# Kernel tuning notes

Measured on AMD Instinct MI355X. Metric: run time of the kernel, lower is better.

## Reference

```python
import jax, jax.numpy as jnp
import numpy as np

Q_DIM = 1024
KV_DIM = 1024
D_ATTN = 1024
N_HEADS = 16
HDIM = D_ATTN // N_HEADS
LOOKBACK = 3
KW = LOOKBACK + 1
SCALE = HDIM ** -0.5

B, LQ, LKV = 4, 4096, 512


def setup_inputs() -> dict:
    key = jax.random.key(0)
    ks = jax.random.split(key, 6)
    q = jax.random.normal(ks[0], (B, LQ, Q_DIM), dtype=jnp.float32)
    kv_src = jax.random.normal(ks[1], (B, LKV, KV_DIM), dtype=jnp.float32)
    seg_id = jnp.sort(jax.random.randint(ks[2], (B, LQ), 0, LKV), axis=-1)
    # Linear weights (torch convention: y = x @ W.T), no bias
    Wq = jax.random.normal(ks[3], (D_ATTN, Q_DIM), dtype=jnp.float32) * (Q_DIM ** -0.5)
    Wkv = jax.random.normal(ks[4], (2 * D_ATTN, KV_DIM), dtype=jnp.float32) * (KV_DIM ** -0.5)
    Wo = jax.random.normal(ks[5], (Q_DIM, D_ATTN), dtype=jnp.float32) * (D_ATTN ** -0.5)
    return {"q": q, "kv_src": kv_src, "seg_id": seg_id, "Wq": Wq, "Wkv": Wkv, "Wo": Wo}


def _split_heads(x):
    # (B, L, D) -> (B, H, L, Dh)
    b, l, _ = x.shape
    return x.reshape(b, l, N_HEADS, HDIM).transpose(0, 2, 1, 3)


def reference(q, kv_src, seg_id, Wq, Wkv, Wo):
    b, lq, _ = q.shape
    lkv = kv_src.shape[1]

    qh = _split_heads(q @ Wq.T)                      # (B,H,Lq,Dh)
    kv = kv_src @ Wkv.T                              # (B,Lkv,2*D)
    k, v = jnp.split(kv, 2, axis=-1)
    kh = _split_heads(k)                             # (B,H,Lkv,Dh)
    vh = _split_heads(v)

    offsets = jnp.arange(KW)                         # (Kw,)
    gather = seg_id[:, :, None] - offsets            # (B,Lq,Kw)
    neg_mask = gather < 0
    gc = jnp.clip(gather, 0, lkv - 1)                # (B,Lq,Kw)

    b_idx = jnp.arange(b)[:, None, None]
    # advanced indexing: (B,Lq,Kw,H,Dh) -> transpose to (B,H,Lq,Kw,Dh)
    k_sel = kh[b_idx, :, gc].transpose(0, 3, 1, 2, 4)
    v_sel = vh[b_idx, :, gc].transpose(0, 3, 1, 2, 4)

    scores = jnp.einsum('bhqd,bhqkd->bhqk', qh, k_sel) * SCALE
    neg_inf = jnp.finfo(scores.dtype).min
    scores = jnp.where(neg_mask[:, None, :, :], neg_inf, scores)
    probs = jax.nn.softmax(scores, axis=-1)
    out = jnp.einsum('bhqk,bhqkd->bhqd', probs, v_sel)   # (B,H,Lq,Dh)
    out = out.transpose(0, 2, 1, 3).reshape(b, lq, D_ATTN)
    return out @ Wo.T                                # (B,Lq,q_dim)
```

## Files before the change

kernel.cpp:

```cpp
#include <hip/hip_runtime.h>
#include <math.h>

#define NH 16
#define HDIM 64
#define D_ATTN 1024
#define KW 4
#define ATT_SCALE 0.125f
#define LKV_C 512
#define LQ_C 4096
#define B_C 4

typedef _Float16 f16;
typedef _Float16 f16x8 __attribute__((ext_vector_type(8)));
typedef _Float16 f16x4 __attribute__((ext_vector_type(4)));
typedef float f32x4 __attribute__((ext_vector_type(4)));

typedef __attribute__((address_space(3))) unsigned int as3_uint;
typedef __attribute__((address_space(1))) const unsigned int as1_uint;

__device__ __forceinline__ void gld_lds16(const f16* g, f16* l) {
    __builtin_amdgcn_global_load_lds((as1_uint*)g, (as3_uint*)l, 16, 0, 0);
}

#define SEG_Q   4194304
#define SEG_KV  (SEG_Q + 524288)
#define SEG_WQ  (SEG_KV + 262144)
#define SEG_WKV (SEG_WQ + 524288)
#define SEG_END (SEG_WKV + 262144)

__global__ __launch_bounds__(256) void split_all(const float* __restrict__ q,
                                                 const float* __restrict__ kv,
                                                 const float* __restrict__ Wq,
                                                 const float* __restrict__ Wkv,
                                                 const float* __restrict__ Wo,
                                                 f16* __restrict__ q_hi,
                                                 f16* __restrict__ kvs_hi,
                                                 f16* __restrict__ Wq_hi,
                                                 f16* __restrict__ Wkv_hi,
                                                 f16* __restrict__ Wo_hi) {
    const int i = blockIdx.x * 256 + threadIdx.x;
    const float* src; f16* dst; int base;
    if (i < SEG_Q)        { src = q;   dst = q_hi;   base = 0; }
    else if (i < SEG_KV)  { src = kv;  dst = kvs_hi; base = SEG_Q; }
    else if (i < SEG_WQ)  { src = Wq;  dst = Wq_hi;  base = SEG_KV; }
    else if (i < SEG_WKV) { src = Wkv; dst = Wkv_hi; base = SEG_WQ; }
    else                  { src = Wo;  dst = Wo_hi;  base = SEG_WKV; }
    const int j = i - base;
    float4 v = ((const float4*)src)[j];
    ((f16x4*)dst)[j] = (f16x4){(f16)v.x, (f16)v.y, (f16)v.z, (f16)v.w};
}

template <typename OT>
__global__ __launch_bounds__(256) void gemm_f16(const f16* __restrict__ A,
                                                const f16* __restrict__ B,
                                                OT* __restrict__ C,
                                                int M, int N, int K) {
    __shared__ f16 smem[2 * 128 * 32];
    f16* sA = smem;
    f16* sB = smem + 4096;

    const int t = threadIdx.x;
    const int w = t >> 6;
    const int lane = t & 63;
    const int bm = blockIdx.y * 128;
    const int bn = blockIdx.x * 128;
    const int wm = (w & 1) * 64;
    const int wn = (w >> 1) * 64;

    f32x4 acc[4][4] = {};

    const int frow = lane & 15;
    const int fchunk = lane >> 4;

    const int srow = t >> 2;
    const int chunk = (t & 3) ^ ((t >> 3) & 3);
    const size_t aoff0 = (size_t)(bm + srow) * K + chunk * 8;
    const size_t aoff1 = (size_t)(bm + 64 + srow) * K + chunk * 8;
    const size_t boff0 = (size_t)(bn + srow) * K + chunk * 8;
    const size_t boff1 = (size_t)(bn + 64 + srow) * K + chunk * 8;
    const unsigned loff0 = (w * 64) * 8;
    const unsigned loff1 = (256 + w * 64) * 8;

    gld_lds16(A + aoff0, sA + loff0);  gld_lds16(A + aoff1, sA + loff1);
    gld_lds16(B + boff0, sB + loff0);  gld_lds16(B + boff1, sB + loff1);

    for (int k0 = 0; k0 < K; k0 += 32) {
        __syncthreads();

        f16x8 a[4], b[4];
        #pragma unroll
        for (int i = 0; i < 4; ++i) {
            const int r = wm + i * 16 + frow;
            a[i] = *(const f16x8*)(sA + r * 32 + (fchunk ^ ((r >> 1) & 3)) * 8);
        }
        #pragma unroll
        for (int j = 0; j < 4; ++j) {
            const int r = wn + j * 16 + frow;
            b[j] = *(const f16x8*)(sB + r * 32 + (fchunk ^ ((r >> 1) & 3)) * 8);
        }

        __syncthreads();

        if (k0 + 32 < K) {
            const int kn = k0 + 32;
            gld_lds16(A + aoff0 + kn, sA + loff0);  gld_lds16(A + aoff1 + kn, sA + loff1);
            gld_lds16(B + boff0 + kn, sB + loff0);  gld_lds16(B + boff1 + kn, sB + loff1);
        }

        #pragma unroll
        for (int i = 0; i < 4; ++i)
            #pragma unroll
            for (int j = 0; j < 4; ++j)
                acc[i][j] = __builtin_amdgcn_mfma_f32_16x16x32_f16(a[i], b[j], acc[i][j], 0, 0, 0);
    }

    const int rbase = bm + wm + (lane >> 4) * 4;
    const int cbase = bn + wn + (lane & 15);
    #pragma unroll
    for (int i = 0; i < 4; ++i)
        #pragma unroll
        for (int j = 0; j < 4; ++j)
            #pragma unroll
            for (int r = 0; r < 4; ++r)
                C[(size_t)(rbase + i * 16 + r) * N + cbase + j * 16] = (OT)acc[i][j][r];
}

__device__ __forceinline__ void stage64(const f16* __restrict__ g, size_t row0,
                                        int K, int kcol, f16* l) {
    const int t = threadIdx.x;
    #pragma unroll
    for (int i = 0; i < 2; ++i) {
        const int idx = i * 256 + t;
        const int r = idx >> 3;
        const int qg = (idx & 7) ^ (r & 7);
        gld_lds16(g + (row0 + r) * (size_t)K + kcol + qg * 8, l + idx * 8);
    }
}

#define BAR __builtin_amdgcn_s_barrier()
#define VM6 asm volatile("s_waitcnt vmcnt(6)" ::: "memory")
#define VM8 asm volatile("s_waitcnt vmcnt(8)" ::: "memory")
#define VM0 asm volatile("s_waitcnt vmcnt(0)" ::: "memory")

#define RD_A(S, mh)                                                         \
    { _Pragma("unroll") for (int mi = 0; mi < 2; ++mi) {                    \
        const f16* p = (S) + ((mh) * 64 + mi * 32 + arow) * 64;             \
        a[0][mi] = *(const f16x8*)(p + q0);                                 \
        a[1][mi] = *(const f16x8*)(p + q1); } }

#define RD_B(S, nh)                                                         \
    { _Pragma("unroll") for (int ni = 0; ni < 2; ++ni) {                    \
        const f16* p = (S) + (((nh) * 2 + ni) * 32 + brow) * 64;            \
        b[0][(nh) * 2 + ni] = *(const f16x8*)(p + q0);                      \
        b[1][(nh) * 2 + ni] = *(const f16x8*)(p + q1); } }

#define QUAD(mh, nh)                                                        \
    { _Pragma("unroll") for (int mi = 0; mi < 2; ++mi)                      \
      _Pragma("unroll") for (int ni = 0; ni < 2; ++ni) {                    \
          f32x4& c = acc[(mh) * 2 + mi][(nh) * 2 + ni];                     \
          c = __builtin_amdgcn_mfma_f32_16x16x32_f16(a[0][mi], b[0][(nh) * 2 + ni], c, 0, 0, 0); \
          c = __builtin_amdgcn_mfma_f32_16x16x32_f16(a[1][mi], b[1][(nh) * 2 + ni], c, 0, 0, 0); \
      } }

#define QUAD2(mh)                                                           \
    { __builtin_amdgcn_s_setprio(1); QUAD(mh, 0); QUAD(mh, 1);              \
      __builtin_amdgcn_s_setprio(0); }

template <typename OT>
__global__ __launch_bounds__(256, 2) void gemm128(const f16* __restrict__ A,
                                                  const f16* __restrict__ B,
                                                  OT* __restrict__ C,
                                                  int M, int N, int K) {
    __shared__ __align__(16) f16 smem[4 * 8192];
    f16* const sA0 = smem;
    f16* const sA1 = smem + 8192;
    f16* const sB0 = smem + 16384;
    f16* const sB1 = smem + 24576;

    const int t = threadIdx.x;
    const int lane = t & 63;
    const int w = t >> 6;
    const int wr = w >> 1;
    const int wc = w & 1;
    const int frow = lane & 15;
    const int fc = lane >> 4;

    const int nbx = N >> 7;
    const int nwg = gridDim.x;
    const int wg = (blockIdx.x & 7) * (nwg >> 3) + (blockIdx.x >> 3);
    const int bm = (wg / nbx) << 7;
    const int bn = (wg % nbx) << 7;

    const int arow = wr * 16 + frow;
    const int brow = wc * 16 + frow;
    const int q0 = (fc ^ (frow & 7)) * 8;
    const int q1 = ((4 + fc) ^ (frow & 7)) * 8;

    f32x4 acc[4][4] = {};
    f16x8 a[2][2], b[2][4];

    stage64(A, bm,      K, 0,  sA0);
    stage64(A, bm + 64, K, 0,  sA0 + 4096);
    stage64(B, bn,      K, 0,  sB0);
    stage64(B, bn + 64, K, 0,  sB0 + 4096);
    stage64(A, bm,      K, 64, sA1);
    stage64(A, bm + 64, K, 64, sA1 + 4096);
    stage64(B, bn,      K, 64, sB1);
    stage64(B, bn + 64, K, 64, sB1 + 4096);
    VM8;
    BAR;

    const int NT = K >> 7;
    for (int it = 0; it < NT; ++it) {
        const bool lastit = (it == NT - 1);
        const int kc1 = (it * 2 + 1) << 6;
        const int kc2 = (it * 2 + 2) << 6;
        const int kc3 = (it * 2 + 3) << 6;

        RD_A(sA0, 0); RD_B(sB0, 0); RD_B(sB0, 1);
        if (it > 0) stage64(A, bm + 64, K, kc1, sA1 + 4096);
        BAR; QUAD2(0); BAR;

        RD_A(sA0, 1);
        if (!lastit) {
            stage64(A, bm,      K, kc2, sA0);
            stage64(B, bn,      K, kc2, sB0);
            stage64(B, bn + 64, K, kc2, sB0 + 4096);
            VM6;
        } else {
            VM0;
        }
        BAR; QUAD2(1); BAR;

        RD_A(sA1, 0); RD_B(sB1, 0); RD_B(sB1, 1);
        if (!lastit) stage64(A, bm + 64, K, kc2, sA0 + 4096);
        BAR; QUAD2(0); BAR;

        RD_A(sA1, 1);
        if (!lastit) {
            stage64(A, bm,      K, kc3, sA1);
            stage64(B, bn,      K, kc3, sB1);
            stage64(B, bn + 64, K, kc3, sB1 + 4096);
            VM6;
        }
        BAR; QUAD2(1); BAR;
    }

    const size_t rb = (size_t)bm + wr * 16 + ((lane >> 4) << 2);
    const int cb = bn + wc * 16 + (lane & 15);
    #pragma unroll
    for (int m = 0; m < 4; ++m)
        #pragma unroll
        for (int n = 0; n < 4; ++n)
            #pragma unroll
            for (int rr = 0; rr < 4; ++rr)
                C[(rb + (m >> 1) * 64 + (m & 1) * 32 + rr) * N + cb + n * 32] =
                    (OT)acc[m][n][rr];
}

__global__ __launch_bounds__(256) void attn_kernel(const f16* __restrict__ qh,
                                                   const f16* __restrict__ kvp,
                                                   const int* __restrict__ seg_id,
                                                   f16* __restrict__ attn_o) {
    const int hg = threadIdx.x >> 6;
    const int lane = threadIdx.x & 63;
    const int r0 = blockIdx.x << 2;
    const int hh = lane >> 4;
    const int s  = lane & 15;
    const int dbase = (hg * 4 + hh) * HDIM + 4 * s;
    const int b = r0 >> 12;
    const f16* kvb = kvp + (size_t)b * LKV_C * (2 * D_ATTN);

    int seg[4];
    float4 q[4];
    #pragma unroll
    for (int i = 0; i < 4; ++i) {
        seg[i] = seg_id[r0 + i];
        f16x4 qv = *(const f16x4*)(qh + (size_t)(r0 + i) * D_ATTN + dbase);
        q[i] = make_float4((float)qv.x, (float)qv.y, (float)qv.z, (float)qv.w);
    }

    float sc[4][KW];
    #pragma unroll
    for (int i = 0; i < 4; ++i)
        #pragma unroll
        for (int w = 0; w < KW; ++w) {
            const int j = seg[i] - w;
            float p = 0.f;
            if (j >= 0) {
                f16x4 k4 = *(const f16x4*)(kvb + (size_t)j * (2 * D_ATTN) + dbase);
                p = q[i].x * (float)k4.x + q[i].y * (float)k4.y +
                    q[i].z * (float)k4.z + q[i].w * (float)k4.w;
            }
            sc[i][w] = p;
        }
    #pragma unroll
    for (int i = 0; i < 4; ++i)
        #pragma unroll
        for (int w = 0; w < KW; ++w) {
            float p = sc[i][w];
            p += __shfl_xor(p, 1);
            p += __shfl_xor(p, 2);
            p += __shfl_xor(p, 4);
            p += __shfl_xor(p, 8);
            sc[i][w] = (seg[i] - w >= 0) ? p * ATT_SCALE : -1e30f;
        }

    #pragma unroll
    for (int i = 0; i < 4; ++i) {
        const float m = fmaxf(fmaxf(sc[i][0], sc[i][1]), fmaxf(sc[i][2], sc[i][3]));
        float e[KW], sum = 0.f;
        #pragma unroll
        for (int w = 0; w < KW; ++w) {
            e[w] = __expf(sc[i][w] - m);
            sum += e[w];
        }
        const float inv = 1.f / sum;

        float4 o = make_float4(0.f, 0.f, 0.f, 0.f);
        #pragma unroll
        for (int w = 0; w < KW; ++w) {
            const int j = seg[i] - w;
            if (j >= 0) {
                f16x4 v4 = *(const f16x4*)(kvb + (size_t)j * (2 * D_ATTN) + D_ATTN + dbase);
                const float c = e[w] * inv;
                o.x = fmaf(c, (float)v4.x, o.x);
                o.y = fmaf(c, (float)v4.y, o.y);
                o.z = fmaf(c, (float)v4.z, o.z);
                o.w = fmaf(c, (float)v4.w, o.w);
            }
        }
        *(f16x4*)(attn_o + (size_t)(r0 + i) * D_ATTN + dbase) =
            (f16x4){(f16)o.x, (f16)o.y, (f16)o.z, (f16)o.w};
    }
}

extern "C" void kernel_launch(void* const* d_in, const int* in_sizes, int n_in,
                              void* d_out, int out_size, void* d_ws, size_t ws_size,
                              hipStream_t stream) {
    const float* q      = (const float*)d_in[0];
    const float* kv_src = (const float*)d_in[1];
    const int*   seg    = (const int*)  d_in[2];
    const float* Wq     = (const float*)d_in[3];
    const float* Wkv    = (const float*)d_in[4];
    const float* Wo     = (const float*)d_in[5];
    float* out = (float*)d_out;

    const int M  = B_C * LQ_C;
    const int Mk = B_C * LKV_C;

    f16* q_hi   = (f16*)d_ws;
    f16* kvs_hi = q_hi   + (size_t)M * D_ATTN;
    f16* Wq_hi  = kvs_hi + (size_t)Mk * 1024;
    f16* Wkv_hi = Wq_hi  + 1024 * 1024;
    f16* Wo_hi  = Wkv_hi + 2048 * 1024;
    f16* kvp    = Wo_hi  + 1024 * 1024;
    f16* attn_o = q_hi;
    f16* qh16   = (f16*)d_out;

    split_all<<<SEG_END / 256, 256, 0, stream>>>(q, kv_src, Wq, Wkv, Wo,
                                                 q_hi, kvs_hi, Wq_hi, Wkv_hi, Wo_hi);

    gemm_f16<f16><<<dim3(2048 / 128, Mk / 128), 256, 0, stream>>>(kvs_hi, Wkv_hi, kvp, Mk, 2048, 1024);
    gemm128<f16><<<(M / 128) * (1024 / 128), 256, 0, stream>>>(q_hi, Wq_hi, qh16, M, 1024, 1024);
    attn_kernel<<<M / 4, 256, 0, stream>>>(qh16, kvp, seg, attn_o);
    gemm128<float><<<(M / 128) * (1024 / 128), 256, 0, stream>>>(attn_o, Wo_hi, out, M, 1024, 1024);
}
```

Baseline: 266.8 us.

## Fuse local-window attention into the Q-projection GEMM epilogue

The Q-projection GEMM now stages its 128x128 output tile in shared memory. It then runs the 4-key windowed attention (dot products via fdot2, softmax, and the weighted V sum) for its two heads directly in the epilogue, writing the attention output to a separate workspace buffer. This removes the separate attention kernel and the round trip of qh through global memory. In exchange, the GEMM blocks carry a longer, latency-bound epilogue with scattered KV gathers. The old path remains as a fallback when the workspace is too small.

```diff
diff --git a/kernel.cpp b/kernel.cpp
--- a/kernel.cpp
+++ b/kernel.cpp
@@ -13,6 +13,7 @@
 typedef _Float16 f16;
 typedef _Float16 f16x8 __attribute__((ext_vector_type(8)));
 typedef _Float16 f16x4 __attribute__((ext_vector_type(4)));
+typedef _Float16 f16x2 __attribute__((ext_vector_type(2)));
 typedef float f32x4 __attribute__((ext_vector_type(4)));
 
 typedef __attribute__((address_space(3))) unsigned int as3_uint;
@@ -20,6 +21,18 @@
 
 __device__ __forceinline__ void gld_lds16(const f16* g, f16* l) {
     __builtin_amdgcn_global_load_lds((as1_uint*)g, (as3_uint*)l, 16, 0, 0);
+}
+
+__device__ __forceinline__ float dot4_f16(f16x4 a, f16x4 b) {
+#if __has_builtin(__builtin_amdgcn_fdot2)
+    f16x2 alo = {a.x, a.y}, ahi = {a.z, a.w};
+    f16x2 blo = {b.x, b.y}, bhi = {b.z, b.w};
+    float p = __builtin_amdgcn_fdot2(alo, blo, 0.f, false);
+    return __builtin_amdgcn_fdot2(ahi, bhi, p, false);
+#else
+    return (float)a.x * (float)b.x + (float)a.y * (float)b.y +
+           (float)a.z * (float)b.z + (float)a.w * (float)b.w;
+#endif
 }
 
 #define SEG_Q   4194304
@@ -166,11 +179,13 @@
     { __builtin_amdgcn_s_setprio(1); QUAD(mh, 0); QUAD(mh, 1);              \
       __builtin_amdgcn_s_setprio(0); }
 
-template <typename OT>
+template <typename OT, bool FUSE>
 __global__ __launch_bounds__(256, 2) void gemm128(const f16* __restrict__ A,
                                                   const f16* __restrict__ B,
                                                   OT* __restrict__ C,
-                                                  int M, int N, int K) {
+                                                  int M, int N, int K,
+                                                  const f16* __restrict__ kvp,
+                                                  const int* __restrict__ seg_id) {
     __shared__ __align__(16) f16 smem[4 * 8192];
     f16* const sA0 = smem;
     f16* const sA1 = smem + 8192;
@@ -246,16 +261,99 @@
         BAR; QUAD2(1); BAR;
     }
 
-    const size_t rb = (size_t)bm + wr * 16 + ((lane >> 4) << 2);
-    const int cb = bn + wc * 16 + (lane & 15);
-    #pragma unroll
-    for (int m = 0; m < 4; ++m)
-        #pragma unroll
-        for (int n = 0; n < 4; ++n)
-            #pragma unroll
-            for (int rr = 0; rr < 4; ++rr)
-                C[(rb + (m >> 1) * 64 + (m & 1) * 32 + rr) * N + cb + n * 32] =
-                    (OT)acc[m][n][rr];
+    if constexpr (!FUSE) {
+        const size_t rb = (size_t)bm + wr * 16 + ((lane >> 4) << 2);
+        const int cb = bn + wc * 16 + (lane & 15);
+        #pragma unroll
+        for (int m = 0; m < 4; ++m)
+            #pragma unroll
+            for (int n = 0; n < 4; ++n)
+                #pragma unroll
+                for (int rr = 0; rr < 4; ++rr)
+                    C[(rb + (m >> 1) * 64 + (m & 1) * 32 + rr) * N + cb + n * 32] =
+                        (OT)acc[m][n][rr];
+    } else {
+        f16* const sQ = smem;
+        __syncthreads();
+        const int lrb = wr * 16 + ((lane >> 4) << 2);
+        const int lcb = wc * 16 + (lane & 15);
+        #pragma unroll
+        for (int m = 0; m < 4; ++m)
+            #pragma unroll
+            for (int n = 0; n < 4; ++n)
+                #pragma unroll
+                for (int rr = 0; rr < 4; ++rr)
+                    sQ[(lrb + (m >> 1) * 64 + (m & 1) * 32 + rr) * 128 + lcb + n * 32] =
+                        (f16)acc[m][n][rr];
+        __syncthreads();
+
+        const int sub = lane >> 5;
+        const int lcol = ((lane >> 4) & 1) * 64 + (lane & 15) * 4;
+        const int bb = bm >> 12;
+        const f16* kvb = kvp + (size_t)bb * LKV_C * (2 * D_ATTN);
+        f16* const Cf = (f16*)C;
+
+        for (int t4 = 0; t4 < 4; ++t4) {
+            int rl[4], sg[4];
+            f16x4 qv[4];
+            #pragma unroll
+            for (int u = 0; u < 4; ++u) {
+                rl[u] = (w << 5) + ((t4 * 4 + u) << 1) + sub;
+                sg[u] = seg_id[bm + rl[u]];
+                qv[u] = *(const f16x4*)(sQ + rl[u] * 128 + lcol);
+            }
+            float sc[4][KW];
+            #pragma unroll
+            for (int u = 0; u < 4; ++u)
+                #pragma unroll
+                for (int wk = 0; wk < KW; ++wk) {
+                    const int j = sg[u] - wk;
+                    float p = 0.f;
+                    if (j >= 0) {
+                        f16x4 k4 = *(const f16x4*)(kvb + (size_t)j * (2 * D_ATTN) + bn + lcol);
+                        p = dot4_f16(qv[u], k4);
+                    }
+                    sc[u][wk] = p;
+                }
+            #pragma unroll
+            for (int u = 0; u < 4; ++u)
+                #pragma unroll
+                for (int wk = 0; wk < KW; ++wk) {
+                    float p = sc[u][wk];
+                    p += __shfl_xor(p, 1);
+                    p += __shfl_xor(p, 2);
+                    p += __shfl_xor(p, 4);
+                    p += __shfl_xor(p, 8);
+                    sc[u][wk] = (sg[u] - wk >= 0) ? p * ATT_SCALE : -1e30f;
+                }
+            #pragma unroll
+            for (int u = 0; u < 4; ++u) {
+                const float mx = fmaxf(fmaxf(sc[u][0], sc[u][1]), fmaxf(sc[u][2], sc[u][3]));
+                float e[KW], sum = 0.f;
+                #pragma unroll
+                for (int wk = 0; wk < KW; ++wk) {
+                    e[wk] = __expf(sc[u][wk] - mx);
+                    sum += e[wk];
+                }
+                const float inv = 1.f / sum;
+                float ox = 0.f, oy = 0.f, oz = 0.f, ow = 0.f;
+                #pragma unroll
+                for (int wk = 0; wk < KW; ++wk) {
+                    const int j = sg[u] - wk;
+                    if (j >= 0) {
+                        f16x4 v4 = *(const f16x4*)(kvb + (size_t)j * (2 * D_ATTN) + D_ATTN + bn + lcol);
+                        const float c = e[wk] * inv;
+                        ox = fmaf(c, (float)v4.x, ox);
+                        oy = fmaf(c, (float)v4.y, oy);
+                        oz = fmaf(c, (float)v4.z, oz);
+                        ow = fmaf(c, (float)v4.w, ow);
+                    }
+                }
+                *(f16x4*)(Cf + (size_t)(bm + rl[u]) * N + bn + lcol) =
+                    (f16x4){(f16)ox, (f16)oy, (f16)oz, (f16)ow};
+            }
+        }
+    }
 }
 
 __global__ __launch_bounds__(256) void attn_kernel(const f16* __restrict__ qh,
@@ -355,14 +453,27 @@
     f16* Wkv_hi = Wq_hi  + 1024 * 1024;
     f16* Wo_hi  = Wkv_hi + 2048 * 1024;
     f16* kvp    = Wo_hi  + 1024 * 1024;
-    f16* attn_o = q_hi;
-    f16* qh16   = (f16*)d_out;
+    f16* attn_sep = kvp  + (size_t)Mk * 2048;
+
+    const size_t need = (size_t)(attn_sep - (f16*)d_ws + (size_t)M * D_ATTN) * sizeof(f16);
 
     split_all<<<SEG_END / 256, 256, 0, stream>>>(q, kv_src, Wq, Wkv, Wo,
                                                  q_hi, kvs_hi, Wq_hi, Wkv_hi, Wo_hi);
 
     gemm_f16<f16><<<dim3(2048 / 128, Mk / 128), 256, 0, stream>>>(kvs_hi, Wkv_hi, kvp, Mk, 2048, 1024);
-    gemm128<f16><<<(M / 128) * (1024 / 128), 256, 0, stream>>>(q_hi, Wq_hi, qh16, M, 1024, 1024);
-    attn_kernel<<<M / 4, 256, 0, stream>>>(qh16, kvp, seg, attn_o);
-    gemm128<float><<<(M / 128) * (1024 / 128), 256, 0, stream>>>(attn_o, Wo_hi, out, M, 1024, 1024);
-}
+
+    if (ws_size >= need) {
+        gemm128<f16, true><<<(M / 128) * (1024 / 128), 256, 0, stream>>>(
+            q_hi, Wq_hi, attn_sep, M, 1024, 1024, kvp, seg);
+        gemm128<float, false><<<(M / 128) * (1024 / 128), 256, 0, stream>>>(
+            attn_sep, Wo_hi, out, M, 1024, 1024, nullptr, nullptr);
+    } else {
+        f16* attn_o = q_hi;
+        f16* qh16   = (f16*)d_out;
+        gemm128<f16, false><<<(M / 128) * (1024 / 128), 256, 0, stream>>>(
+            q_hi, Wq_hi, qh16, M, 1024, 1024, nullptr, nullptr);
+        attn_kernel<<<M / 4, 256, 0, stream>>>(qh16, kvp, seg, attn_o);
+        gemm128<float, false><<<(M / 128) * (1024 / 128), 256, 0, stream>>>(
+            attn_o, Wo_hi, out, M, 1024, 1024, nullptr, nullptr);
+    }
+}
```

Measured after the change: 274.9 us. 3.0% more time.
